# Kernel tuning notes

Hardware: AMD Instinct MI355X
Metric: run time of the kernel (lower is better)

Reference implementation:

```python
import jax, jax.numpy as jnp
import numpy as np

EMB = 256
HID = 512
VOCAB = 32000
SRC_LEN = 50
TRG_LEN = 50
BATCH = 64


def lstm_layer(x, h0, c0, Wih, Whh, b):
    """x: [T,B,in]; h0,c0: [B,H]; Wih: [4H,in]; Whh: [4H,H]; b: [4H].
    PyTorch gate order i,f,g,o. Returns (ys [T,B,H], hT, cT)."""
    def step(carry, xt):
        h, c = carry
        g = xt @ Wih.T + h @ Whh.T + b
        i, f, gg, o = jnp.split(g, 4, axis=-1)
        c = jax.nn.sigmoid(f) * c + jax.nn.sigmoid(i) * jnp.tanh(gg)
        h = jax.nn.sigmoid(o) * jnp.tanh(c)
        return (h, c), h
    (hT, cT), ys = jax.lax.scan(step, (h0, c0), x)
    return ys, hT, cT


def setup_inputs() -> dict:
    key = jax.random.key(0)
    ks = jax.random.split(key, 20)
    s = 0.05
    d = {
        'src': jax.random.randint(ks[0], (SRC_LEN, BATCH), 0, VOCAB),
        'trg': jax.random.randint(ks[1], (TRG_LEN, BATCH), 0, VOCAB),
        'enc_emb': jax.random.normal(ks[2], (VOCAB, EMB), jnp.float32) * s,
        'enc_Wih0': jax.random.normal(ks[3], (4 * HID, EMB), jnp.float32) * s,
        'enc_Whh0': jax.random.normal(ks[4], (4 * HID, HID), jnp.float32) * s,
        'enc_b0': jnp.zeros((4 * HID,), jnp.float32),
        'enc_Wih1': jax.random.normal(ks[5], (4 * HID, HID), jnp.float32) * s,
        'enc_Whh1': jax.random.normal(ks[6], (4 * HID, HID), jnp.float32) * s,
        'enc_b1': jnp.zeros((4 * HID,), jnp.float32),
        'dec_emb': jax.random.normal(ks[7], (VOCAB, EMB), jnp.float32) * s,
        'dec_Wih0': jax.random.normal(ks[8], (4 * HID, EMB), jnp.float32) * s,
        'dec_Whh0': jax.random.normal(ks[9], (4 * HID, HID), jnp.float32) * s,
        'dec_b0': jnp.zeros((4 * HID,), jnp.float32),
        'dec_Wih1': jax.random.normal(ks[10], (4 * HID, HID), jnp.float32) * s,
        'dec_Whh1': jax.random.normal(ks[11], (4 * HID, HID), jnp.float32) * s,
        'dec_b1': jnp.zeros((4 * HID,), jnp.float32),
        'out_W': jax.random.normal(ks[12], (VOCAB, HID), jnp.float32) * s,
        'out_b': jnp.zeros((VOCAB,), jnp.float32),
    }
    return d


def reference(src, trg, enc_emb, enc_Wih0, enc_Whh0, enc_b0, enc_Wih1, enc_Whh1,
              enc_b1, dec_emb, dec_Wih0, dec_Whh0, dec_b0, dec_Wih1, dec_Whh1,
              dec_b1, out_W, out_b):
    B = src.shape[1]
    z = jnp.zeros((B, HID), enc_emb.dtype)
    # Encoder: 2-layer LSTM over src, keep final (h, c) per layer
    xe = enc_emb[src]                                   # [S,B,E]
    y0, h0, c0 = lstm_layer(xe, z, z, enc_Wih0, enc_Whh0, enc_b0)
    _, h1, c1 = lstm_layer(y0, z, z, enc_Wih1, enc_Whh1, enc_b1)
    # Decoder with teacher forcing: inputs are trg[0:T-1]
    xd = dec_emb[trg[:-1]]                              # [T-1,B,E]
    d0, _, _ = lstm_layer(xd, h0, c0, dec_Wih0, dec_Whh0, dec_b0)
    d1, _, _ = lstm_layer(d0, h1, c1, dec_Wih1, dec_Whh1, dec_b1)
    preds = d1 @ out_W.T + out_b                        # [T-1,B,V]
    return preds
```

## Files before the change

kernel.cpp:

```cpp
#include <hip/hip_runtime.h>
#include <hip/hip_bf16.h>

#define BATCH 64
#define HID 512
#define EMB 256
#define VOCAB 32000
#define G4 2048

typedef __attribute__((ext_vector_type(8))) short short8;
typedef __attribute__((ext_vector_type(4))) float f32x4;
typedef __attribute__((ext_vector_type(4))) unsigned short ush4;

__global__ __launch_bounds__(256) void zero_kernel(float* p, int n){
    int i = blockIdx.x*256 + threadIdx.x;
    if (i < n) p[i] = 0.f;
}

__device__ __forceinline__ unsigned short bf16_rne(float x){
    unsigned b = __float_as_uint(x);
    return (unsigned short)((b + 0x7fffu + ((b >> 16) & 1u)) >> 16);
}
__device__ __forceinline__ void split2(float x, unsigned short& h, unsigned short& l){
    h = bf16_rne(x);
    l = bf16_rne(x - __uint_as_float((unsigned)h << 16));
}

__global__ __launch_bounds__(256) void embed_kernel(const int* __restrict__ tok,
                                                    const float* __restrict__ emb,
                                                    float* __restrict__ out, int T){
    int i = blockIdx.x*256 + threadIdx.x;
    int n = T*BATCH*(EMB/4);
    if (i >= n) return;
    int e4 = i % (EMB/4);
    int tb = i / (EMB/4);
    int id = tok[tb];
    reinterpret_cast<float4*>(out)[(size_t)tb*(EMB/4) + e4] =
        reinterpret_cast<const float4*>(emb + (size_t)id*EMB)[e4];
}

__global__ __launch_bounds__(256) void embed_plane_kernel(const int* __restrict__ tok,
                                                          const float* __restrict__ emb,
                                                          unsigned short* __restrict__ hi,
                                                          unsigned short* __restrict__ lo, int T){
    int i = blockIdx.x*256 + threadIdx.x;
    int n = T*BATCH*(EMB/4);
    if (i >= n) return;
    int e4 = i % (EMB/4);
    int tb = i / (EMB/4);
    int id = tok[tb];
    f32x4 v = reinterpret_cast<const f32x4*>(emb + (size_t)id*EMB)[e4];
    ush4 h, l;
    #pragma unroll
    for (int j = 0; j < 4; j++){ unsigned short a,b; split2(v[j], a, b); h[j]=a; l[j]=b; }
    reinterpret_cast<ush4*>(hi)[(size_t)tb*(EMB/4) + e4] = h;
    reinterpret_cast<ush4*>(lo)[(size_t)tb*(EMB/4) + e4] = l;
}

__global__ __launch_bounds__(256) void split_all_kernel(
    const float* __restrict__ outW, unsigned short* __restrict__ Whi,
    const float* __restrict__ w0, unsigned short* __restrict__ w0h, unsigned short* __restrict__ w0l,
    const float* __restrict__ w1, unsigned short* __restrict__ w1h, unsigned short* __restrict__ w1l,
    const float* __restrict__ w2, unsigned short* __restrict__ w2h, unsigned short* __restrict__ w2l,
    const float* __restrict__ w3, unsigned short* __restrict__ w3h, unsigned short* __restrict__ w3l)
{
    int i = blockIdx.x*256 + threadIdx.x;
    if (i < 4096000){
        f32x4 v = reinterpret_cast<const f32x4*>(outW)[i];
        ush4 h;
        #pragma unroll
        for (int j = 0; j < 4; j++) h[j] = bf16_rne(v[j]);
        reinterpret_cast<ush4*>(Whi)[i] = h;
        return;
    }
    i -= 4096000;
    const float* src; unsigned short* dh; unsigned short* dl;
    if (i < 131072){ src = w0; dh = w0h; dl = w0l; }
    else if (i < 131072+262144){ i -= 131072; src = w1; dh = w1h; dl = w1l; }
    else if (i < 131072+262144+131072){ i -= 131072+262144; src = w2; dh = w2h; dl = w2l; }
    else if (i < 131072+262144+131072+262144){ i -= 131072+262144+131072; src = w3; dh = w3h; dl = w3l; }
    else return;
    f32x4 v = reinterpret_cast<const f32x4*>(src)[i];
    ush4 h, l;
    #pragma unroll
    for (int j = 0; j < 4; j++){ unsigned short a,b; split2(v[j], a, b); h[j]=a; l[j]=b; }
    reinterpret_cast<ush4*>(dh)[i] = h;
    reinterpret_cast<ush4*>(dl)[i] = l;
}

template<int KDIM, int NDIM>
__global__ __launch_bounds__(256) void gemm_mfma_split(
    const float* __restrict__ A, const float* __restrict__ B,
    const float* __restrict__ bias, float* __restrict__ C, int M)
{
    constexpr int LS = 40;
    __shared__ unsigned short Ah[128*LS], Al[128*LS], Bh[128*LS], Bl[128*LS];
    const int n0 = blockIdx.x*128, m0 = blockIdx.y*128;
    const int tid  = threadIdx.x;
    const int lane = tid & 63, wid = tid >> 6;
    const int wm = wid >> 1, wn = wid & 1;
    const int srow = tid >> 1, sk = (tid & 1)*16;
    f32x4 acc[4][4] = {};

    for (int k0 = 0; k0 < KDIM; k0 += 32){
        __syncthreads();
        {
            int ar = m0 + srow;
            float xv[16];
            if (ar < M){
                const float4* ap = reinterpret_cast<const float4*>(A + (size_t)ar*KDIM + k0 + sk);
                #pragma unroll
                for (int q = 0; q < 4; q++){
                    float4 v = ap[q];
                    xv[q*4+0]=v.x; xv[q*4+1]=v.y; xv[q*4+2]=v.z; xv[q*4+3]=v.w;
                }
            } else {
                #pragma unroll
                for (int q = 0; q < 16; q++) xv[q] = 0.f;
            }
            #pragma unroll
            for (int q = 0; q < 16; q++){
                unsigned short h,l; split2(xv[q], h, l);
                Ah[srow*LS + sk + q] = h;
                Al[srow*LS + sk + q] = l;
            }
        }
        {
            int br = n0 + srow;
            const float4* bp = reinterpret_cast<const float4*>(B + (size_t)br*KDIM + k0 + sk);
            #pragma unroll
            for (int q = 0; q < 4; q++){
                float4 v = bp[q];
                float xs[4] = {v.x, v.y, v.z, v.w};
                #pragma unroll
                for (int j = 0; j < 4; j++){
                    unsigned short h,l; split2(xs[j], h, l);
                    Bh[srow*LS + sk + q*4 + j] = h;
                    Bl[srow*LS + sk + q*4 + j] = l;
                }
            }
        }
        __syncthreads();
        const int fr = lane & 15, fk = (lane >> 4)*8;
        short8 a_h[4], a_l[4], b_h[4], b_l[4];
        #pragma unroll
        for (int mi = 0; mi < 4; mi++){
            int row = wm*64 + mi*16 + fr;
            a_h[mi] = *reinterpret_cast<const short8*>(&Ah[row*LS + fk]);
            a_l[mi] = *reinterpret_cast<const short8*>(&Al[row*LS + fk]);
        }
        #pragma unroll
        for (int nj = 0; nj < 4; nj++){
            int rowb = wn*64 + nj*16 + fr;
            b_h[nj] = *reinterpret_cast<const short8*>(&Bh[rowb*LS + fk]);
            b_l[nj] = *reinterpret_cast<const short8*>(&Bl[rowb*LS + fk]);
        }
        #pragma unroll
        for (int mi = 0; mi < 4; mi++)
            #pragma unroll
            for (int nj = 0; nj < 4; nj++){
                acc[mi][nj] = __builtin_amdgcn_mfma_f32_16x16x32_bf16(a_h[mi], b_h[nj], acc[mi][nj], 0,0,0);
                acc[mi][nj] = __builtin_amdgcn_mfma_f32_16x16x32_bf16(a_h[mi], b_l[nj], acc[mi][nj], 0,0,0);
                acc[mi][nj] = __builtin_amdgcn_mfma_f32_16x16x32_bf16(a_l[mi], b_h[nj], acc[mi][nj], 0,0,0);
            }
    }
    const int fr = lane & 15, fq = lane >> 4;
    #pragma unroll
    for (int nj = 0; nj < 4; nj++){
        int col = n0 + wn*64 + nj*16 + fr;
        float bv = bias[col];
        #pragma unroll
        for (int mi = 0; mi < 4; mi++){
            int rbase = m0 + wm*64 + mi*16 + fq*4;
            #pragma unroll
            for (int j = 0; j < 4; j++){
                int row = rbase + j;
                if (row < M)
                    __builtin_nontemporal_store(acc[mi][nj][j] + bv, &C[(size_t)row*NDIM + col]);
            }
        }
    }
}

__device__ __forceinline__ void gll16(const unsigned short* g, unsigned short* l){
    __builtin_amdgcn_global_load_lds(
        (const __attribute__((address_space(1))) unsigned int*)g,
        (__attribute__((address_space(3))) unsigned int*)l, 16, 0, 0);
}

template<int KDIM, int NDIM, int NTN>
__device__ __forceinline__ void gemm_gll_body(
    const unsigned short* __restrict__ Ahi, const unsigned short* __restrict__ Alo,
    const unsigned short* __restrict__ Bhi, const unsigned short* __restrict__ Blo,
    const float* __restrict__ bias, float* __restrict__ C, int M,
    int bid_raw, int total)
{
    __shared__ unsigned short P[4][128*32];
    const int q = total >> 3, r8 = total & 7;
    const int xcd = bid_raw & 7, idx = bid_raw >> 3;
    const int lid = (xcd < r8 ? xcd*(q+1) : r8*(q+1) + (xcd - r8)*q) + idx;
    const int m0 = (lid / NTN)*128, n0 = (lid % NTN)*128;

    const int tid  = threadIdx.x;
    const int lane = tid & 63, wid = tid >> 6;
    const int wm = wid >> 1, wn = wid & 1;

    const unsigned short* gsrc = (wid == 0) ? Ahi : (wid == 1) ? Alo
                               : (wid == 2) ? Bhi : Blo;
    const int row0 = (wid < 2) ? m0 : n0;
    const unsigned short* gbase = gsrc + (size_t)(row0 + (lane >> 2))*KDIM
                                       + 8*((lane & 3) ^ ((lane >> 3) & 3));
    unsigned short* lbase = &P[wid][0];

    f32x4 acc[4][4] = {};

    for (int k0 = 0; k0 < KDIM; k0 += 32){
        __syncthreads();
        #pragma unroll
        for (int i = 0; i < 8; i++)
            gll16(gbase + k0 + (size_t)i*16*KDIM, lbase + i*512);
        __syncthreads();

        const int fr = lane & 15, fkq = lane >> 4;
        const int swz = 8*(fkq ^ ((fr >> 1) & 3));
        short8 a_h[4], a_l[4], b_h[4], b_l[4];
        #pragma unroll
        for (int mi = 0; mi < 4; mi++){
            int row = wm*64 + mi*16 + fr;
            a_h[mi] = *reinterpret_cast<const short8*>(&P[0][row*32 + swz]);
            a_l[mi] = *reinterpret_cast<const short8*>(&P[1][row*32 + swz]);
        }
        #pragma unroll
        for (int nj = 0; nj < 4; nj++){
            int row = wn*64 + nj*16 + fr;
            b_h[nj] = *reinterpret_cast<const short8*>(&P[2][row*32 + swz]);
            b_l[nj] = *reinterpret_cast<const short8*>(&P[3][row*32 + swz]);
        }
        #pragma unroll
        for (int mi = 0; mi < 4; mi++)
            #pragma unroll
            for (int nj = 0; nj < 4; nj++){
                acc[mi][nj] = __builtin_amdgcn_mfma_f32_16x16x32_bf16(a_h[mi], b_h[nj], acc[mi][nj], 0,0,0);
                acc[mi][nj] = __builtin_amdgcn_mfma_f32_16x16x32_bf16(a_l[mi], b_h[nj], acc[mi][nj], 0,0,0);
                acc[mi][nj] = __builtin_amdgcn_mfma_f32_16x16x32_bf16(a_h[mi], b_l[nj], acc[mi][nj], 0,0,0);
            }
    }
    const int fr = lane & 15, fq = lane >> 4;
    #pragma unroll
    for (int nj = 0; nj < 4; nj++){
        int col = n0 + wn*64 + nj*16 + fr;
        float bv = bias[col];
        #pragma unroll
        for (int mi = 0; mi < 4; mi++){
            int rbase = m0 + wm*64 + mi*16 + fq*4;
            #pragma unroll
            for (int j = 0; j < 4; j++){
                int row = rbase + j;
                if (row < M)
                    __builtin_nontemporal_store(acc[mi][nj][j] + bv, &C[(size_t)row*NDIM + col]);
            }
        }
    }
}

template<int KDIM, int NDIM, int NTN>
__global__ __launch_bounds__(256) void gemm_planes_gll(
    const unsigned short* Ahi, const unsigned short* Alo,
    const unsigned short* Bhi, const unsigned short* Blo,
    const float* bias, float* C, int M)
{
    gemm_gll_body<KDIM, NDIM, NTN>(Ahi, Alo, Bhi, Blo, bias, C, M,
                                   blockIdx.x, gridDim.x);
}

template<int KDIM, int NDIM, int NTN>
__device__ __forceinline__ void gemm_final_body(
    const unsigned short* __restrict__ Ahi,
    const unsigned short* __restrict__ Bhi,
    const float* __restrict__ bias, float* __restrict__ C, int M,
    int bid, int total, unsigned* __restrict__ gprog, int T)
{
    __shared__ unsigned short Ah[256*32];
    __shared__ unsigned short Bh[128*32];
    const int q = total >> 3, r8 = total & 7;
    const int xcd = bid & 7, idx = bid >> 3;
    const int lid = (xcd < r8 ? xcd*(q+1) : r8*(q+1) + (xcd - r8)*q) + idx;
    const int m0 = (lid / NTN)*256, n0 = (lid % NTN)*128;

    const int tid  = threadIdx.x;
    const int lane = tid & 63, wid = tid >> 6;
    const int wm = wid >> 1, wn = wid & 1;

    if (gprog){
        int thresh = 4*(lid / NTN) + 4;
        if (thresh > T) thresh = T;
        if (tid < 64){
            unsigned spins = 0; bool done = false;
            while (!done && spins < (1u<<14)){
                unsigned v = (unsigned)thresh;
                if (tid < 8)
                    v = __hip_atomic_load(&gprog[tid], __ATOMIC_RELAXED, __HIP_MEMORY_SCOPE_AGENT);
                done = (bool)__all((int)(v >= (unsigned)thresh));
                spins++;
                if (!done) __builtin_amdgcn_s_sleep(8);
            }
        }
        __syncthreads();
    }

    const bool stager = (wid < 6);
    const unsigned short* gsrc = (wid < 4) ? Ahi : Bhi;
    const int grow0 = (wid < 4) ? (m0 + wid*64) : (n0 + (wid - 4)*64);
    const unsigned short* gbase = gsrc + (size_t)(grow0 + (lane >> 2))*KDIM
                                       + 8*((lane & 3) ^ ((lane >> 3) & 3));
    unsigned short* lbase = (wid < 4) ? (Ah + wid*64*32) : (Bh + (wid - 4)*64*32);

    f32x4 acc[4][4] = {};

    for (int k0 = 0; k0 < KDIM; k0 += 32){
        __syncthreads();
        if (stager){
            #pragma unroll
            for (int i = 0; i < 4; i++)
                gll16(gbase + k0 + (size_t)i*16*KDIM, lbase + i*512);
        }
        __syncthreads();

        const int fr = lane & 15, fkq = lane >> 4;
        const int swz = 8*(fkq ^ ((fr >> 1) & 3));
        short8 a_h[4], b_h[4];
        #pragma unroll
        for (int nj = 0; nj < 4; nj++){
            int row = wn*64 + nj*16 + fr;
            b_h[nj] = *reinterpret_cast<const short8*>(&Bh[row*32 + swz]);
        }
        #pragma unroll
        for (int mi = 0; mi < 4; mi++){
            int row = wm*64 + mi*16 + fr;
            a_h[mi] = *reinterpret_cast<const short8*>(&Ah[row*32 + swz]);
        }
        #pragma unroll
        for (int mi = 0; mi < 4; mi++)
            #pragma unroll
            for (int nj = 0; nj < 4; nj++)
                acc[mi][nj] = __builtin_amdgcn_mfma_f32_16x16x32_bf16(a_h[mi], b_h[nj], acc[mi][nj], 0,0,0);
    }
    const int fr = lane & 15, fq = lane >> 4;
    #pragma unroll
    for (int nj = 0; nj < 4; nj++){
        int col = n0 + wn*64 + nj*16 + fr;
        float bv = bias[col];
        #pragma unroll
        for (int mi = 0; mi < 4; mi++){
            int rbase = m0 + wm*64 + mi*16 + fq*4;
            #pragma unroll
            for (int j = 0; j < 4; j++){
                int row = rbase + j;
                if (row < M)
                    __builtin_nontemporal_store(acc[mi][nj][j] + bv, &C[(size_t)row*NDIM + col]);
            }
        }
    }
}

template<int KDIM, int NDIM, int NTN>
__global__ __launch_bounds__(512) void gemm_planes_256w8(
    const unsigned short* Ahi, const unsigned short* Bhi,
    const float* bias, float* C, int M)
{
    gemm_final_body<KDIM, NDIM, NTN>(Ahi, Bhi, bias, C, M,
                                     blockIdx.x, gridDim.x, nullptr, 0);
}

__device__ __forceinline__ void lstm_body(
    const float* __restrict__ Xp, const float* __restrict__ Whh,
    const float* __restrict__ hinit, const float* __restrict__ cinit,
    float* __restrict__ ys, float* __restrict__ cfin,
    int T, unsigned* __restrict__ flagbase, int bx,
    unsigned short* __restrict__ phi, unsigned short* __restrict__ plo)
{
    constexpr int WS = 520;
    __shared__ unsigned short hH[8*WS], hL[8*WS];
    __shared__ __align__(16) float red[4*544 + 128];
    __shared__ unsigned short zbuf[8];

    const int bc  = bx & 7, hc = bx >> 3;
    const int hid0 = hc*16;
    const int tid = threadIdx.x;
    const int lane = tid & 63, kc = tid >> 6;
    const int fr = lane & 15, fkq = lane >> 4;
    unsigned* myflag = flagbase + (size_t)(bc*32 + hc)*16;

    if (tid < 8) zbuf[tid] = 0;

    short8 ah[4][4], al[4][4];
    #pragma unroll
    for (int m = 0; m < 4; m++){
        const float* wr = Whh + (size_t)(m*HID + hid0 + fr)*HID;
        #pragma unroll
        for (int s = 0; s < 4; s++){
            int k0 = kc*128 + s*32 + fkq*8;
            f32x4 v0 = *reinterpret_cast<const f32x4*>(wr + k0);
            f32x4 v1 = *reinterpret_cast<const f32x4*>(wr + k0 + 4);
            short8 h8, l8;
            float xv[8] = {v0[0],v0[1],v0[2],v0[3],v1[0],v1[1],v1[2],v1[3]};
            #pragma unroll
            for (int j = 0; j < 8; j++){
                unsigned short hh, ll; split2(xv[j], hh, ll);
                h8[j] = (short)hh; l8[j] = (short)ll;
            }
            ah[m][s] = h8; al[m][s] = l8;
        }
    }

    const int ub = tid >> 4;
    const int uh = tid & 15;
    float creg = 0.f;
    if (tid < 128) creg = cinit[(size_t)(bc*8 + ub)*HID + hid0 + uh];

    const size_t hbase = (size_t)bc*8*HID;
    const float* xprow = Xp + (size_t)(bc*8 + ub)*G4 + hid0 + uh;

    float xn0=0.f, xn1=0.f, xn2=0.f, xn3=0.f;
    if (tid < 128){
        const float* xpr = xprow;
        xn0 = xpr[0]; xn1 = xpr[512]; xn2 = xpr[1024]; xn3 = xpr[1536];
    }

    for (int t = 0; t < T; t++){
        {
            const f32x4* hsrc = reinterpret_cast<const f32x4*>(
                (t == 0) ? (hinit + hbase) : (ys + (size_t)(t-1)*BATCH*HID + hbase));
            #pragma unroll
            for (int j = 0; j < 4; j++){
                int fidx = tid + j*256;
                f32x4 v = hsrc[fidx];
                int e   = fidx*4;
                int row = e >> 9, col = e & 511;
                ush4 h, l;
                #pragma unroll
                for (int qq = 0; qq < 4; qq++){ unsigned short a,b; split2(v[qq], a, b); h[qq]=a; l[qq]=b; }
                *reinterpret_cast<ush4*>(&hH[row*WS + col]) = h;
                *reinterpret_cast<ush4*>(&hL[row*WS + col]) = l;
            }
        }
        __syncthreads();

        {
            f32x4 acc4[4] = {};
            const bool breal = fr < 8;
            #pragma unroll
            for (int s = 0; s < 4; s++){
                int k0 = kc*128 + s*32 + fkq*8;
                short8 bh = breal ? *reinterpret_cast<const short8*>(&hH[fr*WS + k0])
                                  : *reinterpret_cast<const short8*>(zbuf);
                short8 bl = breal ? *reinterpret_cast<const short8*>(&hL[fr*WS + k0])
                                  : *reinterpret_cast<const short8*>(zbuf);
                #pragma unroll
                for (int m = 0; m < 4; m++){
                    acc4[m] = __builtin_amdgcn_mfma_f32_16x16x32_bf16(ah[m][s], bh, acc4[m], 0,0,0);
                    acc4[m] = __builtin_amdgcn_mfma_f32_16x16x32_bf16(ah[m][s], bl, acc4[m], 0,0,0);
                    acc4[m] = __builtin_amdgcn_mfma_f32_16x16x32_bf16(al[m][s], bh, acc4[m], 0,0,0);
                }
            }
            const int b = lane & 15;
            if (b < 8){
                #pragma unroll
                for (int m = 0; m < 4; m++)
                    *reinterpret_cast<f32x4*>(&red[kc*544 + b*68 + m*16 + (lane >> 4)*4]) = acc4[m];
            }
        }
        __syncthreads();

        if (tid < 64){
            #pragma unroll
            for (int b = 0; b < 8; b++)
                red[b*68 + tid] = red[b*68 + tid] + red[544 + b*68 + tid]
                               + red[1088 + b*68 + tid] + red[1632 + b*68 + tid];
        }
        __syncthreads();

        if (tid < 128){
            float gi = red[ub*68 + 0*16 + uh] + xn0;
            float gf = red[ub*68 + 1*16 + uh] + xn1;
            float gg = red[ub*68 + 2*16 + uh] + xn2;
            float go = red[ub*68 + 3*16 + uh] + xn3;
            float si = 1.f/(1.f + expf(-gi));
            float sf = 1.f/(1.f + expf(-gf));
            float so = 1.f/(1.f + expf(-go));
            float tg = tanhf(gg);
            float c = sf*creg + si*tg;
            creg = c;
            float hval = so * tanhf(c);
            red[2176 + tid] = hval;
            if (phi){
                unsigned short hh, ll; split2(hval, hh, ll);
                size_t poff = (size_t)t*BATCH*HID + (size_t)(bc*8 + ub)*HID + hid0 + uh;
                phi[poff] = hh; plo[poff] = ll;
            }
            if (t < T-1){
                const float* xpr = xprow + (size_t)(t+1)*BATCH*G4;
                xn0 = xpr[0]; xn1 = xpr[512]; xn2 = xpr[1024]; xn3 = xpr[1536];
            }
        }
        __syncthreads();

        if (tid < 64){
            if (tid < 32){
                f32x4 v = *reinterpret_cast<const f32x4*>(&red[2176 + tid*4]);
                const f32x4* addr = reinterpret_cast<const f32x4*>(
                    ys + (size_t)t*BATCH*HID
                       + (size_t)(bc*8 + (tid >> 2))*HID + hid0 + (tid & 3)*4);
                asm volatile("global_store_dwordx4 %0, %1, off sc0 sc1"
                             :: "v"(addr), "v"(v) : "memory");
            }
            if (t < T-1){
                asm volatile("s_waitcnt vmcnt(0)" ::: "memory");
                if (tid == 0)
                    __hip_atomic_store(myflag, (unsigned)(t+1),
                                       __ATOMIC_RELAXED, __HIP_MEMORY_SCOPE_AGENT);
                const unsigned tgt = (unsigned)(t+1);
                unsigned* fp = flagbase + (size_t)(bc*32 + (tid & 31))*16;
                unsigned spins = 0;
                bool done = false;
                while (!done && spins < (1u<<20)){
                    unsigned v = tgt;
                    if (tid < 32)
                        v = __hip_atomic_load(fp, __ATOMIC_RELAXED, __HIP_MEMORY_SCOPE_AGENT);
                    done = (bool)__all((int)(v >= tgt));
                    spins++;
                }
            }
        }
        __syncthreads();
    }

    if (tid < 128)
        cfin[(size_t)(bc*8 + ub)*HID + hid0 + uh] = creg;
}

__global__ __launch_bounds__(256, 2) void lstm_layer_k(
    const float* Xp, const float* Whh, const float* hinit, const float* cinit,
    float* ys, float* cfin, int T, unsigned* flagbase,
    unsigned short* phi, unsigned short* plo)
{
    lstm_body(Xp, Whh, hinit, cinit, ys, cfin, T, flagbase, blockIdx.x, phi, plo);
}

__global__ __launch_bounds__(256, 2) void lstm_dual_k(
    const float* Xp0, const float* Whh0, const float* hi0, const float* ci0,
    float* ys0, float* cf0, int T0, unsigned* fl0,
    unsigned short* phi0, unsigned short* plo0,
    const float* Xp1, const float* Whh1, const float* hi1, const float* ci1,
    float* ys1, float* cf1, int T1, unsigned* fl1,
    unsigned short* phi1, unsigned short* plo1)
{
    const int role = blockIdx.x >> 8;
    const int bx = blockIdx.x & 255;
    if (role == 0)
        lstm_body(Xp0, Whh0, hi0, ci0, ys0, cf0, T0, fl0, bx, phi0, plo0);
    else
        lstm_body(Xp1, Whh1, hi1, ci1, ys1, cf1, T1, fl1, bx, phi1, plo1);
}

__global__ __launch_bounds__(256, 2) void lstm_gemm_k(
    const float* Xp, const float* Whh, const float* hinit, const float* cinit,
    float* ys, float* cfin, int T, unsigned* flagbase,
    unsigned short* phi, unsigned short* plo,
    const unsigned short* gAhi, const unsigned short* gAlo,
    const unsigned short* gBhi, const unsigned short* gBlo,
    const float* gbias, float* gC, int gM, int gTotal)
{
    if ((int)blockIdx.x < 256)
        lstm_body(Xp, Whh, hinit, cinit, ys, cfin, T, flagbase, blockIdx.x, phi, plo);
    else
        gemm_gll_body<EMB, G4, 16>(gAhi, gAlo, gBhi, gBlo, gbias, gC, gM,
                                   blockIdx.x - 256, gTotal);
}

__device__ __forceinline__ void lstm_body8(
    const float* __restrict__ Xp, const float* __restrict__ Whh,
    const float* __restrict__ hinit, const float* __restrict__ cinit,
    float* __restrict__ ys, float* __restrict__ cfin,
    int T, unsigned* __restrict__ flagbase, int bx,
    unsigned short* __restrict__ phi, unsigned short* __restrict__ plo,
    unsigned* __restrict__ gprog)
{
    constexpr int WS = 520;
    __shared__ unsigned short hH[8*WS], hL[8*WS];
    __shared__ __align__(16) float red[8*544 + 128];
    __shared__ unsigned short zbuf[8];

    const int bc = bx & 7, hc = bx >> 3;
    const int hid0 = hc*16;
    const int tid = threadIdx.x;
    const int lane = tid & 63, kc = tid >> 6;
    const int fr = lane & 15, fkq = lane >> 4;
    unsigned* myflag = flagbase + (size_t)(bc*32 + hc)*16;

    if (tid < 8) zbuf[tid] = 0;

    short8 ah[4][2], al[4][2];
    #pragma unroll
    for (int m = 0; m < 4; m++){
        const float* wr = Whh + (size_t)(m*HID + hid0 + fr)*HID;
        #pragma unroll
        for (int s = 0; s < 2; s++){
            int k0 = kc*64 + s*32 + fkq*8;
            f32x4 v0 = *reinterpret_cast<const f32x4*>(wr + k0);
            f32x4 v1 = *reinterpret_cast<const f32x4*>(wr + k0 + 4);
            short8 h8, l8;
            float xv[8] = {v0[0],v0[1],v0[2],v0[3],v1[0],v1[1],v1[2],v1[3]};
            #pragma unroll
            for (int j = 0; j < 8; j++){
                unsigned short hh, ll; split2(xv[j], hh, ll);
                h8[j] = (short)hh; l8[j] = (short)ll;
            }
            ah[m][s] = h8; al[m][s] = l8;
        }
    }

    const int ub = tid >> 4;
    const int uh = tid & 15;
    float creg = 0.f;
    if (tid < 128) creg = cinit[(size_t)(bc*8 + ub)*HID + hid0 + uh];

    const size_t hbase = (size_t)bc*8*HID;
    const float* xprow = Xp + (size_t)(bc*8 + ub)*G4 + hid0 + uh;

    float xn0=0.f, xn1=0.f, xn2=0.f, xn3=0.f;
    if (tid < 128){
        const float* xpr = xprow;
        xn0 = xpr[0]; xn1 = xpr[512]; xn2 = xpr[1024]; xn3 = xpr[1536];
    }

    for (int t = 0; t < T; t++){
        {
            const f32x4* hsrc = reinterpret_cast<const f32x4*>(
                (t == 0) ? (hinit + hbase) : (ys + (size_t)(t-1)*BATCH*HID + hbase));
            #pragma unroll
            for (int j = 0; j < 2; j++){
                int fidx = tid + j*512;
                f32x4 v = hsrc[fidx];
                int e   = fidx*4;
                int row = e >> 9, col = e & 511;
                ush4 h, l;
                #pragma unroll
                for (int qq = 0; qq < 4; qq++){ unsigned short a,b; split2(v[qq], a, b); h[qq]=a; l[qq]=b; }
                *reinterpret_cast<ush4*>(&hH[row*WS + col]) = h;
                *reinterpret_cast<ush4*>(&hL[row*WS + col]) = l;
            }
        }
        __syncthreads();

        {
            f32x4 acc4[4] = {};
            const bool breal = fr < 8;
            #pragma unroll
            for (int s = 0; s < 2; s++){
                int k0 = kc*64 + s*32 + fkq*8;
                short8 bh = breal ? *reinterpret_cast<const short8*>(&hH[fr*WS + k0])
                                  : *reinterpret_cast<const short8*>(zbuf);
                short8 bl = breal ? *reinterpret_cast<const short8*>(&hL[fr*WS + k0])
                                  : *reinterpret_cast<const short8*>(zbuf);
                #pragma unroll
                for (int m = 0; m < 4; m++){
                    acc4[m] = __builtin_amdgcn_mfma_f32_16x16x32_bf16(ah[m][s], bh, acc4[m], 0,0,0);
                    acc4[m] = __builtin_amdgcn_mfma_f32_16x16x32_bf16(ah[m][s], bl, acc4[m], 0,0,0);
                    acc4[m] = __builtin_amdgcn_mfma_f32_16x16x32_bf16(al[m][s], bh, acc4[m], 0,0,0);
                }
            }
            const int b = lane & 15;
            if (b < 8){
                #pragma unroll
                for (int m = 0; m < 4; m++)
                    *reinterpret_cast<f32x4*>(&red[kc*544 + b*68 + m*16 + (lane >> 4)*4]) = acc4[m];
            }
        }
        __syncthreads();

        if (tid < 64){
            #pragma unroll
            for (int b = 0; b < 8; b++){
                float v = red[b*68 + tid];
                #pragma unroll
                for (int s = 1; s < 8; s++) v += red[s*544 + b*68 + tid];
                red[b*68 + tid] = v;
            }
        }
        __syncthreads();

        if (tid < 128){
            float gi = red[ub*68 + 0*16 + uh] + xn0;
            float gf = red[ub*68 + 1*16 + uh] + xn1;
            float gg = red[ub*68 + 2*16 + uh] + xn2;
            float go = red[ub*68 + 3*16 + uh] + xn3;
            float si = 1.f/(1.f + expf(-gi));
            float sf = 1.f/(1.f + expf(-gf));
            float so = 1.f/(1.f + expf(-go));
            float tg = tanhf(gg);
            float c = sf*creg + si*tg;
            creg = c;
            red[4352 + tid] = so * tanhf(c);
            if (t < T-1){
                const float* xpr = xprow + (size_t)(t+1)*BATCH*G4;
                xn0 = xpr[0]; xn1 = xpr[512]; xn2 = xpr[1024]; xn3 = xpr[1536];
            }
        }
        __syncthreads();

        if (tid < 64){
            if (tid < 32){
                f32x4 v = *reinterpret_cast<const f32x4*>(&red[4352 + tid*4]);
                size_t eoff = (size_t)t*BATCH*HID
                            + (size_t)(bc*8 + (tid >> 2))*HID + hid0 + (tid & 3)*4;
                const f32x4* addr = reinterpret_cast<const f32x4*>(ys + eoff);
                asm volatile("global_store_dwordx4 %0, %1, off sc0 sc1"
                             :: "v"(addr), "v"(v) : "memory");
                if (phi){
                    ush4 hh, ll;
                    #pragma unroll
                    for (int j = 0; j < 4; j++){ unsigned short a,b; split2(v[j], a, b); hh[j]=a; ll[j]=b; }
                    const ush4* pa = reinterpret_cast<const ush4*>(phi + eoff);
                    const ush4* pb = reinterpret_cast<const ush4*>(plo + eoff);
                    asm volatile("global_store_dwordx2 %0, %1, off sc0 sc1"
                                 :: "v"(pa), "v"(hh) : "memory");
                    asm volatile("global_store_dwordx2 %0, %1, off sc0 sc1"
                                 :: "v"(pb), "v"(ll) : "memory");
                }
            }
            asm volatile("s_waitcnt vmcnt(0)" ::: "memory");
            if (tid == 0)
                __hip_atomic_store(myflag, (unsigned)(t+1),
                                   __ATOMIC_RELAXED, __HIP_MEMORY_SCOPE_AGENT);
            if (t < T-1){
                const unsigned tgt = (unsigned)(t+1);
                unsigned* fp = flagbase + (size_t)(bc*32 + (tid & 31))*16;
                unsigned spins = 0;
                bool done = false;
                while (!done && spins < (1u<<20)){
                    unsigned v = tgt;
                    if (tid < 32)
                        v = __hip_atomic_load(fp, __ATOMIC_RELAXED, __HIP_MEMORY_SCOPE_AGENT);
                    done = (bool)__all((int)(v >= tgt));
                    spins++;
                }
                if (gprog && hc == 0 && tid == 0)
                    __hip_atomic_store(&gprog[bc], tgt,
                                       __ATOMIC_RELAXED, __HIP_MEMORY_SCOPE_AGENT);
            }
        }
        __syncthreads();
    }

    if (tid < 128)
        cfin[(size_t)(bc*8 + ub)*HID + hid0 + uh] = creg;

    if (gprog && hc == 0 && tid < 64){
        const unsigned tgt = (unsigned)T;
        unsigned* fp = flagbase + (size_t)(bc*32 + (tid & 31))*16;
        unsigned spins = 0;
        bool done = false;
        while (!done && spins < (1u<<20)){
            unsigned v = tgt;
            if (tid < 32)
                v = __hip_atomic_load(fp, __ATOMIC_RELAXED, __HIP_MEMORY_SCOPE_AGENT);
            done = (bool)__all((int)(v >= tgt));
            spins++;
        }
        if (tid == 0)
            __hip_atomic_store(&gprog[bc], tgt,
                               __ATOMIC_RELAXED, __HIP_MEMORY_SCOPE_AGENT);
    }
}

__global__ __launch_bounds__(512, 2) void lstm_final_k(
    const float* Xp, const float* Whh, const float* hinit, const float* cinit,
    float* ys, float* cfin, int T, unsigned* flagbase,
    unsigned short* phi, unsigned short* plo, unsigned* gprog,
    const unsigned short* gA, const unsigned short* gB,
    const float* gbias, float* gC, int gM, int gTotal)
{
    if ((int)blockIdx.x < 256)
        lstm_body8(Xp, Whh, hinit, cinit, ys, cfin, T, flagbase, blockIdx.x,
                   phi, plo, gprog);
    else
        gemm_final_body<HID, VOCAB, 250>(gA, gB, gbias, gC, gM,
                                         blockIdx.x - 256, gTotal, gprog, T);
}

extern "C" void kernel_launch(void* const* d_in, const int* in_sizes, int n_in,
                              void* d_out, int out_size, void* d_ws, size_t ws_size,
                              hipStream_t stream) {
    const int*   src      = (const int*)  d_in[0];
    const int*   trg      = (const int*)  d_in[1];
    const float* enc_emb  = (const float*)d_in[2];
    const float* enc_Wih0 = (const float*)d_in[3];
    const float* enc_Whh0 = (const float*)d_in[4];
    const float* enc_b0   = (const float*)d_in[5];
    const float* enc_Wih1 = (const float*)d_in[6];
    const float* enc_Whh1 = (const float*)d_in[7];
    const float* enc_b1   = (const float*)d_in[8];
    const float* dec_emb  = (const float*)d_in[9];
    const float* dec_Wih0 = (const float*)d_in[10];
    const float* dec_Whh0 = (const float*)d_in[11];
    const float* dec_b0   = (const float*)d_in[12];
    const float* dec_Wih1 = (const float*)d_in[13];
    const float* dec_Whh1 = (const float*)d_in[14];
    const float* dec_b1   = (const float*)d_in[15];
    const float* out_W    = (const float*)d_in[16];
    const float* out_b    = (const float*)d_in[17];

    float* ob = (float*)d_out;
    float* Xp   = ob;
    float* xe   = ob + (size_t)6553600;
    float* xd   = ob + (size_t)7372800;
    float* eys0 = ob + (size_t)8175616;
    float* eys1 = ob + (size_t)9814016;
    float* dys0 = ob + (size_t)11452416;
    float* Xp2  = ob + (size_t)13058048;

    float* ws = (float*)d_ws;
    float* dys1 = ws;
    float* c0   = ws + (size_t)1605632;
    float* c1   = ws + (size_t)1638400;
    float* hz   = ws + (size_t)1671168;
    unsigned* flags = (unsigned*)(ws + (size_t)1703936);
    unsigned* gprog = ((unsigned*)(ws + (size_t)1703936)) - 16;
    unsigned short* Whi = (unsigned short*)(ws + (size_t)1720320);
    unsigned short* Wlo = Whi + (size_t)16384000;
    unsigned short* Ahi = Wlo + (size_t)16384000;
    unsigned short* Alo = Ahi + (size_t)1703936;
    unsigned short* eW0h = Alo  + (size_t)1703936;
    unsigned short* eW0l = eW0h + (size_t)524288;
    unsigned short* eW1h = eW0l + (size_t)524288;
    unsigned short* eW1l = eW1h + (size_t)1048576;
    unsigned short* dW0h = eW1l + (size_t)1048576;
    unsigned short* dW0l = dW0h + (size_t)524288;
    unsigned short* dW1h = dW0l + (size_t)524288;
    unsigned short* dW1l = dW1h + (size_t)1048576;
    unsigned short* XAh  = dW1l + (size_t)1048576;
    unsigned short* XAl  = XAh  + (size_t)1638400;
    const size_t end_xp = (size_t)1720320*4 +
        2*((size_t)16384000*2 + (size_t)1703936*2 + (size_t)524288*4 +
           (size_t)1048576*4 + (size_t)1638400*2);
    float* Xp3 = (float*)((char*)d_ws + end_xp);
    const size_t end_fused = end_xp + (size_t)3136*2048*4;
    const bool xp_ok    = (ws_size >= end_xp);
    const bool fused_ok = (ws_size >= end_fused);

    {
        int n = 3*BATCH*HID + 4*4096;
        zero_kernel<<<(n+255)/256, 256, 0, stream>>>(c0, n);
    }

    if (xp_ok){
        split_all_kernel<<<(4882432 + 255)/256, 256, 0, stream>>>(
            out_W, Whi,
            enc_Wih0, eW0h, eW0l,  enc_Wih1, eW1h, eW1l,
            dec_Wih0, dW0h, dW0l,  dec_Wih1, dW1h, dW1l);
        embed_plane_kernel<<<(50*BATCH*(EMB/4)+255)/256, 256, 0, stream>>>(src, enc_emb, XAh, XAl, 50);
        embed_plane_kernel<<<(49*BATCH*(EMB/4)+255)/256, 256, 0, stream>>>(trg, dec_emb, Ahi, Alo, 49);
    } else {
        embed_kernel<<<(50*BATCH*(EMB/4)+255)/256, 256, 0, stream>>>(src, enc_emb, xe, 50);
        embed_kernel<<<(49*BATCH*(EMB/4)+255)/256, 256, 0, stream>>>(trg, dec_emb, xd, 49);
    }

    dim3 xgrid(G4/128, 25);

    if (xp_ok)
        gemm_planes_gll<EMB, G4, 16><<<400, 256, 0, stream>>>(XAh, XAl, eW0h, eW0l, enc_b0, Xp, 3200);
    else
        gemm_mfma_split<EMB, G4><<<xgrid, 256, 0, stream>>>(xe, enc_Wih0, enc_b0, Xp, 3200);

    if (xp_ok){
        lstm_gemm_k<<<656, 256, 0, stream>>>(
            Xp, enc_Whh0, hz, hz, eys0, c0, 50, flags + 0, XAh, XAl,
            Ahi, Alo, dW0h, dW0l, dec_b0, Xp2, 3136, 400);
    } else {
        lstm_layer_k<<<256, 256, 0, stream>>>(Xp, enc_Whh0, hz, hz, eys0, c0, 50, flags + 0,
                                              nullptr, nullptr);
        gemm_mfma_split<EMB, G4><<<xgrid, 256, 0, stream>>>(xd, dec_Wih0, dec_b0, Xp2, 3136);
    }

    if (xp_ok)
        gemm_planes_gll<HID, G4, 16><<<400, 256, 0, stream>>>(XAh, XAl, eW1h, eW1l, enc_b1, Xp, 3200);
    else
        gemm_mfma_split<HID, G4><<<xgrid, 256, 0, stream>>>(eys0, enc_Wih1, enc_b1, Xp, 3200);

    lstm_dual_k<<<512, 256, 0, stream>>>(
        Xp,  enc_Whh1, hz,                          hz, eys1, c1, 50, flags + 4096,  nullptr, nullptr,
        Xp2, dec_Whh0, eys0 + (size_t)49*BATCH*HID, c0, dys0, c0, 49, flags + 8192,
        xp_ok ? XAh : nullptr, XAl);

    float* XpD1 = fused_ok ? Xp3 : Xp;
    if (xp_ok)
        gemm_planes_gll<HID, G4, 16><<<400, 256, 0, stream>>>(XAh, XAl, dW1h, dW1l, dec_b1, XpD1, 3136);
    else
        gemm_mfma_split<HID, G4><<<xgrid, 256, 0, stream>>>(dys0, dec_Wih1, dec_b1, XpD1, 3136);

    if (fused_ok){
        lstm_final_k<<<256 + 3250, 512, 0, stream>>>(
            Xp3, dec_Whh1, eys1 + (size_t)49*BATCH*HID, c1, dys1, c1, 49, flags + 12288,
            Ahi, Alo, gprog,
            Ahi, Whi, out_b, (float*)d_out, 3136, 3250);
    } else if (xp_ok){
        lstm_layer_k<<<256, 256, 0, stream>>>(XpD1, dec_Whh1, eys1 + (size_t)49*BATCH*HID, c1,
                                              dys1, c1, 49, flags + 12288, Ahi, Alo);
        gemm_planes_256w8<HID, VOCAB, 250><<<13*250, 512, 0, stream>>>(
            Ahi, Whi, out_b, (float*)d_out, 3136);
    } else {
        lstm_layer_k<<<256, 256, 0, stream>>>(XpD1, dec_Whh1, eys1 + (size_t)49*BATCH*HID, c1,
                                              dys1, c1, 49, flags + 12288, nullptr, nullptr);
        gemm_mfma_split<HID, VOCAB><<<dim3(VOCAB/128, 25), 256, 0, stream>>>(
            dys1, out_W, out_b, (float*)d_out, 3136);
    }
}
```

Measured before the change: 996.2 us.

## Overlap out_W bf16 conversion with dual LSTM and shrink fused final kernel tiles

```diff
diff --git a/kernel.cpp b/kernel.cpp
--- a/kernel.cpp
+++ b/kernel.cpp
@@ -56,23 +56,13 @@
     reinterpret_cast<ush4*>(lo)[(size_t)tb*(EMB/4) + e4] = l;
 }
 
-__global__ __launch_bounds__(256) void split_all_kernel(
-    const float* __restrict__ outW, unsigned short* __restrict__ Whi,
+__global__ __launch_bounds__(256) void split_wih_kernel(
     const float* __restrict__ w0, unsigned short* __restrict__ w0h, unsigned short* __restrict__ w0l,
     const float* __restrict__ w1, unsigned short* __restrict__ w1h, unsigned short* __restrict__ w1l,
     const float* __restrict__ w2, unsigned short* __restrict__ w2h, unsigned short* __restrict__ w2l,
     const float* __restrict__ w3, unsigned short* __restrict__ w3h, unsigned short* __restrict__ w3l)
 {
     int i = blockIdx.x*256 + threadIdx.x;
-    if (i < 4096000){
-        f32x4 v = reinterpret_cast<const f32x4*>(outW)[i];
-        ush4 h;
-        #pragma unroll
-        for (int j = 0; j < 4; j++) h[j] = bf16_rne(v[j]);
-        reinterpret_cast<ush4*>(Whi)[i] = h;
-        return;
-    }
-    i -= 4096000;
     const float* src; unsigned short* dh; unsigned short* dl;
     if (i < 131072){ src = w0; dh = w0h; dl = w0l; }
     else if (i < 131072+262144){ i -= 131072; src = w1; dh = w1h; dl = w1l; }
@@ -273,39 +263,22 @@
 }
 
 template<int KDIM, int NDIM, int NTN>
-__device__ __forceinline__ void gemm_final_body(
+__global__ __launch_bounds__(512) void gemm_planes_256w8(
     const unsigned short* __restrict__ Ahi,
     const unsigned short* __restrict__ Bhi,
-    const float* __restrict__ bias, float* __restrict__ C, int M,
-    int bid, int total, unsigned* __restrict__ gprog, int T)
+    const float* __restrict__ bias, float* __restrict__ C, int M)
 {
     __shared__ unsigned short Ah[256*32];
     __shared__ unsigned short Bh[128*32];
+    const int total = gridDim.x;
     const int q = total >> 3, r8 = total & 7;
-    const int xcd = bid & 7, idx = bid >> 3;
+    const int xcd = blockIdx.x & 7, idx = blockIdx.x >> 3;
     const int lid = (xcd < r8 ? xcd*(q+1) : r8*(q+1) + (xcd - r8)*q) + idx;
     const int m0 = (lid / NTN)*256, n0 = (lid % NTN)*128;
 
     const int tid  = threadIdx.x;
     const int lane = tid & 63, wid = tid >> 6;
     const int wm = wid >> 1, wn = wid & 1;
-
-    if (gprog){
-        int thresh = 4*(lid / NTN) + 4;
-        if (thresh > T) thresh = T;
-        if (tid < 64){
-            unsigned spins = 0; bool done = false;
-            while (!done && spins < (1u<<14)){
-                unsigned v = (unsigned)thresh;
-                if (tid < 8)
-                    v = __hip_atomic_load(&gprog[tid], __ATOMIC_RELAXED, __HIP_MEMORY_SCOPE_AGENT);
-                done = (bool)__all((int)(v >= (unsigned)thresh));
-                spins++;
-                if (!done) __builtin_amdgcn_s_sleep(8);
-            }
-        }
-        __syncthreads();
-    }
 
     const bool stager = (wid < 6);
     const unsigned short* gsrc = (wid < 4) ? Ahi : Bhi;
@@ -360,15 +333,6 @@
             }
         }
     }
-}
-
-template<int KDIM, int NDIM, int NTN>
-__global__ __launch_bounds__(512) void gemm_planes_256w8(
-    const unsigned short* Ahi, const unsigned short* Bhi,
-    const float* bias, float* C, int M)
-{
-    gemm_final_body<KDIM, NDIM, NTN>(Ahi, Bhi, bias, C, M,
-                                     blockIdx.x, gridDim.x, nullptr, 0);
 }
 
 __device__ __forceinline__ void lstm_body(
@@ -552,14 +516,24 @@
     unsigned short* phi0, unsigned short* plo0,
     const float* Xp1, const float* Whh1, const float* hi1, const float* ci1,
     float* ys1, float* cf1, int T1, unsigned* fl1,
-    unsigned short* phi1, unsigned short* plo1)
+    unsigned short* phi1, unsigned short* plo1,
+    const float* outW, unsigned short* Whi)
 {
     const int role = blockIdx.x >> 8;
     const int bx = blockIdx.x & 255;
     if (role == 0)
         lstm_body(Xp0, Whh0, hi0, ci0, ys0, cf0, T0, fl0, bx, phi0, plo0);
-    else
+    else if (role == 1)
         lstm_body(Xp1, Whh1, hi1, ci1, ys1, cf1, T1, fl1, bx, phi1, plo1);
+    else if (outW){
+        for (int i = bx*256 + threadIdx.x; i < 4096000; i += 65536){
+            f32x4 v = reinterpret_cast<const f32x4*>(outW)[i];
+            ush4 h;
+            #pragma unroll
+            for (int j = 0; j < 4; j++) h[j] = bf16_rne(v[j]);
+            reinterpret_cast<ush4*>(Whi)[i] = h;
+        }
+    }
 }
 
 __global__ __launch_bounds__(256, 2) void lstm_gemm_k(
@@ -577,20 +551,22 @@
                                    blockIdx.x - 256, gTotal);
 }
 
-__device__ __forceinline__ void lstm_body8(
+
+__device__ void lstm_body_pc(
+    char* smem,
     const float* __restrict__ Xp, const float* __restrict__ Whh,
     const float* __restrict__ hinit, const float* __restrict__ cinit,
     float* __restrict__ ys, float* __restrict__ cfin,
     int T, unsigned* __restrict__ flagbase, int bx,
-    unsigned short* __restrict__ phi, unsigned short* __restrict__ plo,
-    unsigned* __restrict__ gprog)
+    unsigned short* __restrict__ phi, unsigned* __restrict__ gprog)
 {
     constexpr int WS = 520;
-    __shared__ unsigned short hH[8*WS], hL[8*WS];
-    __shared__ __align__(16) float red[8*544 + 128];
-    __shared__ unsigned short zbuf[8];
-
-    const int bc = bx & 7, hc = bx >> 3;
+    unsigned short* hH = (unsigned short*)smem;
+    unsigned short* hL = hH + 8*WS;
+    float* red = (float*)(smem + 16640);
+    unsigned short* zbuf = (unsigned short*)(smem + 25856);
+
+    const int bc  = bx & 7, hc = bx >> 3;
     const int hid0 = hc*16;
     const int tid = threadIdx.x;
     const int lane = tid & 63, kc = tid >> 6;
@@ -599,13 +575,13 @@
 
     if (tid < 8) zbuf[tid] = 0;
 
-    short8 ah[4][2], al[4][2];
+    short8 ah[4][4], al[4][4];
     #pragma unroll
     for (int m = 0; m < 4; m++){
         const float* wr = Whh + (size_t)(m*HID + hid0 + fr)*HID;
         #pragma unroll
-        for (int s = 0; s < 2; s++){
-            int k0 = kc*64 + s*32 + fkq*8;
+        for (int s = 0; s < 4; s++){
+            int k0 = kc*128 + s*32 + fkq*8;
             f32x4 v0 = *reinterpret_cast<const f32x4*>(wr + k0);
             f32x4 v1 = *reinterpret_cast<const f32x4*>(wr + k0 + 4);
             short8 h8, l8;
@@ -638,8 +614,8 @@
             const f32x4* hsrc = reinterpret_cast<const f32x4*>(
                 (t == 0) ? (hinit + hbase) : (ys + (size_t)(t-1)*BATCH*HID + hbase));
             #pragma unroll
-            for (int j = 0; j < 2; j++){
-                int fidx = tid + j*512;
+            for (int j = 0; j < 4; j++){
+                int fidx = tid + j*256;
                 f32x4 v = hsrc[fidx];
                 int e   = fidx*4;
                 int row = e >> 9, col = e & 511;
@@ -656,8 +632,8 @@
             f32x4 acc4[4] = {};
             const bool breal = fr < 8;
             #pragma unroll
-            for (int s = 0; s < 2; s++){
-                int k0 = kc*64 + s*32 + fkq*8;
+            for (int s = 0; s < 4; s++){
+                int k0 = kc*128 + s*32 + fkq*8;
                 short8 bh = breal ? *reinterpret_cast<const short8*>(&hH[fr*WS + k0])
                                   : *reinterpret_cast<const short8*>(zbuf);
                 short8 bl = breal ? *reinterpret_cast<const short8*>(&hL[fr*WS + k0])
@@ -680,12 +656,9 @@
 
         if (tid < 64){
             #pragma unroll
-            for (int b = 0; b < 8; b++){
-                float v = red[b*68 + tid];
-                #pragma unroll
-                for (int s = 1; s < 8; s++) v += red[s*544 + b*68 + tid];
-                red[b*68 + tid] = v;
-            }
+            for (int b = 0; b < 8; b++)
+                red[b*68 + tid] = red[b*68 + tid] + red[544 + b*68 + tid]
+                               + red[1088 + b*68 + tid] + red[1632 + b*68 + tid];
         }
         __syncthreads();
 
@@ -700,7 +673,7 @@
             float tg = tanhf(gg);
             float c = sf*creg + si*tg;
             creg = c;
-            red[4352 + tid] = so * tanhf(c);
+            red[2176 + tid] = so * tanhf(c);
             if (t < T-1){
                 const float* xpr = xprow + (size_t)(t+1)*BATCH*G4;
                 xn0 = xpr[0]; xn1 = xpr[512]; xn2 = xpr[1024]; xn3 = xpr[1536];
@@ -710,23 +683,18 @@
 
         if (tid < 64){
             if (tid < 32){
-                f32x4 v = *reinterpret_cast<const f32x4*>(&red[4352 + tid*4]);
+                f32x4 v = *reinterpret_cast<const f32x4*>(&red[2176 + tid*4]);
                 size_t eoff = (size_t)t*BATCH*HID
                             + (size_t)(bc*8 + (tid >> 2))*HID + hid0 + (tid & 3)*4;
                 const f32x4* addr = reinterpret_cast<const f32x4*>(ys + eoff);
                 asm volatile("global_store_dwordx4 %0, %1, off sc0 sc1"
                              :: "v"(addr), "v"(v) : "memory");
-                if (phi){
-                    ush4 hh, ll;
-                    #pragma unroll
-                    for (int j = 0; j < 4; j++){ unsigned short a,b; split2(v[j], a, b); hh[j]=a; ll[j]=b; }
-                    const ush4* pa = reinterpret_cast<const ush4*>(phi + eoff);
-                    const ush4* pb = reinterpret_cast<const ush4*>(plo + eoff);
-                    asm volatile("global_store_dwordx2 %0, %1, off sc0 sc1"
-                                 :: "v"(pa), "v"(hh) : "memory");
-                    asm volatile("global_store_dwordx2 %0, %1, off sc0 sc1"
-                                 :: "v"(pb), "v"(ll) : "memory");
-                }
+                ush4 hh;
+                #pragma unroll
+                for (int j = 0; j < 4; j++) hh[j] = bf16_rne(v[j]);
+                const ush4* pa = reinterpret_cast<const ush4*>(phi + eoff);
+                asm volatile("global_store_dwordx2 %0, %1, off sc0 sc1"
+                             :: "v"(pa), "v"(hh) : "memory");
             }
             asm volatile("s_waitcnt vmcnt(0)" ::: "memory");
             if (tid == 0)
@@ -744,7 +712,7 @@
                     done = (bool)__all((int)(v >= tgt));
                     spins++;
                 }
-                if (gprog && hc == 0 && tid == 0)
+                if (hc == 0 && tid == 0)
                     __hip_atomic_store(&gprog[bc], tgt,
                                        __ATOMIC_RELAXED, __HIP_MEMORY_SCOPE_AGENT);
             }
@@ -755,7 +723,7 @@
     if (tid < 128)
         cfin[(size_t)(bc*8 + ub)*HID + hid0 + uh] = creg;
 
-    if (gprog && hc == 0 && tid < 64){
+    if (hc == 0 && tid < 64){
         const unsigned tgt = (unsigned)T;
         unsigned* fp = flagbase + (size_t)(bc*32 + (tid & 31))*16;
         unsigned spins = 0;
@@ -773,19 +741,111 @@
     }
 }
 
-__global__ __launch_bounds__(512, 2) void lstm_final_k(
+template<int KDIM, int NDIM, int NTN>
+__device__ void gemm_final128_body(
+    char* smem,
+    const unsigned short* __restrict__ Ahi,
+    const unsigned short* __restrict__ Bhi,
+    const float* __restrict__ bias, float* __restrict__ C, int M,
+    int bid, int total, unsigned* __restrict__ gprog, int T)
+{
+    unsigned short* Ah = (unsigned short*)smem;
+    unsigned short* Bh = Ah + 128*32;
+    const int q = total >> 3, r8 = total & 7;
+    const int xcd = bid & 7, idx = bid >> 3;
+    const int lid = (xcd < r8 ? xcd*(q+1) : r8*(q+1) + (xcd - r8)*q) + idx;
+    const int m0 = (lid / NTN)*128, n0 = (lid % NTN)*128;
+
+    const int tid  = threadIdx.x;
+    const int lane = tid & 63, wid = tid >> 6;
+    const int wm = wid >> 1, wn = wid & 1;
+
+    {
+        int thresh = 2*(lid / NTN) + 2;
+        if (thresh > T) thresh = T;
+        if (tid < 64){
+            unsigned spins = 0; bool done = false;
+            while (!done && spins < (1u<<13)){
+                unsigned v = (unsigned)thresh;
+                if (tid < 8)
+                    v = __hip_atomic_load(&gprog[tid], __ATOMIC_RELAXED, __HIP_MEMORY_SCOPE_AGENT);
+                done = (bool)__all((int)(v >= (unsigned)thresh));
+                spins++;
+                if (!done) __builtin_amdgcn_s_sleep(8);
+            }
+        }
+        __syncthreads();
+    }
+
+    const bool stager = (wid == 0) || (wid == 2);
+    const unsigned short* gsrc = (wid < 2) ? Ahi : Bhi;
+    const int row0 = (wid < 2) ? m0 : n0;
+    const unsigned short* gbase = gsrc + (size_t)(row0 + (lane >> 2))*KDIM
+                                       + 8*((lane & 3) ^ ((lane >> 3) & 3));
+    unsigned short* lbase = (wid < 2) ? Ah : Bh;
+
+    f32x4 acc[4][4] = {};
+
+    for (int k0 = 0; k0 < KDIM; k0 += 32){
+        __syncthreads();
+        if (stager){
+            #pragma unroll
+            for (int i = 0; i < 8; i++)
+                gll16(gbase + k0 + (size_t)i*16*KDIM, lbase + i*512);
+        }
+        __syncthreads();
+
+        const int fr = lane & 15, fkq = lane >> 4;
+        const int swz = 8*(fkq ^ ((fr >> 1) & 3));
+        short8 a_h[4], b_h[4];
+        #pragma unroll
+        for (int mi = 0; mi < 4; mi++){
+            int row = wm*64 + mi*16 + fr;
+            a_h[mi] = *reinterpret_cast<const short8*>(&Ah[row*32 + swz]);
+        }
+        #pragma unroll
+        for (int nj = 0; nj < 4; nj++){
+            int row = wn*64 + nj*16 + fr;
+            b_h[nj] = *reinterpret_cast<const short8*>(&Bh[row*32 + swz]);
+        }
+        #pragma unroll
+        for (int mi = 0; mi < 4; mi++)
+            #pragma unroll
+            for (int nj = 0; nj < 4; nj++)
+                acc[mi][nj] = __builtin_amdgcn_mfma_f32_16x16x32_bf16(a_h[mi], b_h[nj], acc[mi][nj], 0,0,0);
+    }
+    const int fr = lane & 15, fq = lane >> 4;
+    #pragma unroll
+    for (int nj = 0; nj < 4; nj++){
+        int col = n0 + wn*64 + nj*16 + fr;
+        float bv = bias[col];
+        #pragma unroll
+        for (int mi = 0; mi < 4; mi++){
+            int rbase = m0 + wm*64 + mi*16 + fq*4;
+            #pragma unroll
+            for (int j = 0; j < 4; j++){
+                int row = rbase + j;
+                if (row < M)
+                    __builtin_nontemporal_store(acc[mi][nj][j] + bv, &C[(size_t)row*NDIM + col]);
+            }
+        }
+    }
+}
+
+__global__ __launch_bounds__(256, 2) void lstm_final_k(
     const float* Xp, const float* Whh, const float* hinit, const float* cinit,
     float* ys, float* cfin, int T, unsigned* flagbase,
-    unsigned short* phi, unsigned short* plo, unsigned* gprog,
+    unsigned short* phi, unsigned* gprog,
     const unsigned short* gA, const unsigned short* gB,
     const float* gbias, float* gC, int gM, int gTotal)
 {
+    __shared__ __align__(16) char fsmem[25888];
     if ((int)blockIdx.x < 256)
-        lstm_body8(Xp, Whh, hinit, cinit, ys, cfin, T, flagbase, blockIdx.x,
-                   phi, plo, gprog);
+        lstm_body_pc(fsmem, Xp, Whh, hinit, cinit, ys, cfin, T, flagbase,
+                     blockIdx.x, phi, gprog);
     else
-        gemm_final_body<HID, VOCAB, 250>(gA, gB, gbias, gC, gM,
-                                         blockIdx.x - 256, gTotal, gprog, T);
+        gemm_final128_body<HID, VOCAB, 250>(fsmem, gA, gB, gbias, gC, gM,
+                                            blockIdx.x - 256, gTotal, gprog, T);
 }
 
 extern "C" void kernel_launch(void* const* d_in, const int* in_sizes, int n_in,
@@ -854,8 +914,7 @@
     }
 
     if (xp_ok){
-        split_all_kernel<<<(4882432 + 255)/256, 256, 0, stream>>>(
-            out_W, Whi,
+        split_wih_kernel<<<(786432 + 255)/256, 256, 0, stream>>>(
             enc_Wih0, eW0h, eW0l,  enc_Wih1, eW1h, eW1l,
             dec_Wih0, dW0h, dW0l,  dec_Wih1, dW1h, dW1l);
         embed_plane_kernel<<<(50*BATCH*(EMB/4)+255)/256, 256, 0, stream>>>(src, enc_emb, XAh, XAl, 50);
@@ -887,10 +946,11 @@
     else
         gemm_mfma_split<HID, G4><<<xgrid, 256, 0, stream>>>(eys0, enc_Wih1, enc_b1, Xp, 3200);
 
-    lstm_dual_k<<<512, 256, 0, stream>>>(
+    lstm_dual_k<<<768, 256, 0, stream>>>(
         Xp,  enc_Whh1, hz,                          hz, eys1, c1, 50, flags + 4096,  nullptr, nullptr,
         Xp2, dec_Whh0, eys0 + (size_t)49*BATCH*HID, c0, dys0, c0, 49, flags + 8192,
-        xp_ok ? XAh : nullptr, XAl);
+        xp_ok ? XAh : nullptr, XAl,
+        xp_ok ? out_W : nullptr, Whi);
 
     float* XpD1 = fused_ok ? Xp3 : Xp;
     if (xp_ok)
@@ -899,10 +959,10 @@
         gemm_mfma_split<HID, G4><<<xgrid, 256, 0, stream>>>(dys0, dec_Wih1, dec_b1, XpD1, 3136);
 
     if (fused_ok){
-        lstm_final_k<<<256 + 3250, 512, 0, stream>>>(
+        lstm_final_k<<<256 + 6250, 256, 0, stream>>>(
             Xp3, dec_Whh1, eys1 + (size_t)49*BATCH*HID, c1, dys1, c1, 49, flags + 12288,
-            Ahi, Alo, gprog,
-            Ahi, Whi, out_b, (float*)d_out, 3136, 3250);
+            Ahi, gprog,
+            Ahi, Whi, out_b, (float*)d_out, 3136, 6250);
     } else if (xp_ok){
         lstm_layer_k<<<256, 256, 0, stream>>>(XpD1, dec_Whh1, eys1 + (size_t)49*BATCH*HID, c1,
                                               dys1, c1, 49, flags + 12288, Ahi, Alo);
```

Result: slower. 1.023 ms (+2.7%).
